# Optimization experiments

Measured on AMD Instinct MI355X. Metric: run time of the kernel, lower is better.

The kernel has to match this reference:

```python
import jax, jax.numpy as jnp
import numpy as np

N, D, M = 100000, 128, 2048


def setup_inputs() -> dict:
    key = jax.random.key(0)
    k1, k2, k3, k4 = jax.random.split(key, 4)
    X = jax.random.normal(k1, (N, D), dtype=jnp.float32)
    Y = jax.random.normal(k2, (N, 1), dtype=jnp.float32)
    centers = jax.random.normal(k3, (M, D), dtype=jnp.float32)
    # alpha is a buffer produced by an inner Falkon solve; use small random values
    alpha = jax.random.normal(k4, (M, 1), dtype=jnp.float32) * 0.01
    sigma = jnp.asarray(1.0, dtype=jnp.float32)     # Gaussian kernel lengthscale (nn.Parameter)
    penalty = jnp.asarray(5.0, dtype=jnp.float32)   # lambda = exp(-penalty)
    return {"X": X, "Y": Y, "centers": centers, "alpha": alpha,
            "sigma": sigma, "penalty": penalty}


def _rbf_mmv(A, B, v, sigma):
    # Gaussian (RBF) kernel mat-vec: exp(-||a-b||^2 / (2 sigma^2)) @ v
    # A:[n,d], B:[m,d], v:[m,1] -> [n,1]
    a2 = jnp.sum(A * A, axis=-1, keepdims=True)          # [n,1]
    b2 = jnp.sum(B * B, axis=-1, keepdims=True).T        # [1,m]
    sq = a2 + b2 - 2.0 * (A @ B.T)                       # [n,m] squared distances
    Kmat = jnp.exp(-sq / (2.0 * sigma * sigma))
    return Kmat @ v


def reference(X, Y, centers, alpha, sigma, penalty):
    # loss = mean((K_NM @ alpha - Y)^2) + exp(-penalty) * alpha^T K_MM alpha
    preds = _rbf_mmv(X, centers, alpha, sigma)                     # [N,1]
    loss = jnp.mean((preds - Y) ** 2)
    pen = jnp.exp(-penalty)
    reg = pen * (alpha.T @ _rbf_mmv(centers, centers, alpha, sigma))  # [1,1]
    total = loss + reg[0, 0]
    return total, preds
```

## Files before the change

### kernel.cpp

```cpp
#include <hip/hip_runtime.h>
#include <stdint.h>

typedef short short8 __attribute__((ext_vector_type(8)));
typedef float f32x4 __attribute__((ext_vector_type(4)));

#define TILE 128

__device__ __forceinline__ unsigned short f32_to_bf16(float f) {
    uint32_t u = __builtin_bit_cast(uint32_t, f);
    u += 0x7FFFu + ((u >> 16) & 1u);
    return (unsigned short)(u >> 16);
}
__device__ __forceinline__ float bf16_to_f32(unsigned short h) {
    return __builtin_bit_cast(float, (uint32_t)h << 16);
}

__global__ void prep_kernel(const float* __restrict__ C,
                            const float* __restrict__ alpha,
                            const float* __restrict__ sigma,
                            unsigned short* __restrict__ Bp,
                            float2* __restrict__ cw)
{
    const int t = threadIdx.x;
    const int g = blockIdx.x;
    const int r = t >> 4;
    const int c16 = t & 15;
    const int R = g * 16 + r;

    const float4* src = (const float4*)(C + (size_t)R * 128 + c16 * 8);
    float4 va = src[0], vb = src[1];
    unsigned short h[8];
    h[0] = f32_to_bf16(va.x); h[1] = f32_to_bf16(va.y);
    h[2] = f32_to_bf16(va.z); h[3] = f32_to_bf16(va.w);
    h[4] = f32_to_bf16(vb.x); h[5] = f32_to_bf16(vb.y);
    h[6] = f32_to_bf16(vb.z); h[7] = f32_to_bf16(vb.w);
    float ss = 0.f;
    #pragma unroll
    for (int k = 0; k < 8; ++k) {
        float f = bf16_to_f32(h[k]);
        ss = fmaf(f, f, ss);
    }
    uint4 pk;
    pk.x = (uint32_t)h[0] | ((uint32_t)h[1] << 16);
    pk.y = (uint32_t)h[2] | ((uint32_t)h[3] << 16);
    pk.z = (uint32_t)h[4] | ((uint32_t)h[5] << 16);
    pk.w = (uint32_t)h[6] | ((uint32_t)h[7] << 16);
    *reinterpret_cast<uint4*>(Bp + (size_t)g * 2048 + c16 * 128 + r * 8) = pk;

    ss += __shfl_xor(ss, 1);
    ss += __shfl_xor(ss, 2);
    ss += __shfl_xor(ss, 4);
    ss += __shfl_xor(ss, 8);
    if (c16 == 0) {
        float sig = sigma[0];
        float q = 0.7213475204444817f / (sig * sig);
        cw[R] = make_float2(ss * q, alpha[R]);
    }
}

__global__ __launch_bounds__(256, 2)
void fused_kernel(const float* __restrict__ X, int N,
                  const float* __restrict__ Yv,
                  const unsigned short* __restrict__ Bp,
                  const float2* __restrict__ cw,
                  const float* __restrict__ alpha,
                  const float* __restrict__ sigma,
                  int nA, int nMt,
                  float* __restrict__ preds_out,
                  float* __restrict__ accLoss,
                  float* __restrict__ accReg)
{
    __shared__ __align__(16) unsigned short ldsA[16384];
    __shared__ float a2p[TILE][2];
    __shared__ float predbuf[TILE][2];

    const int t    = threadIdx.x;
    const int lane = t & 63;
    const int wid  = t >> 6;
    const int wr   = wid >> 1;
    const int wc   = wid & 1;
    const int l15  = lane & 15;
    const int quad = lane >> 4;

    const float sig = sigma[0];
    const float q  = 0.7213475204444817f / (sig * sig);
    const float q2 = 2.0f * q;

    const bool regmode = (int)blockIdx.x >= nA;
    int rowbase;
    float rowterm[4][4];
    const unsigned short* aGlob = nullptr;

    if (!regmode) {
        rowbase = blockIdx.x * TILE;
        const int r_   = t >> 1;
        const int half = t & 1;
        const int grow = rowbase + r_;
        unsigned short* dstbase = ldsA + (r_ >> 4) * 2048 + (r_ & 15) * 8;
        float ss = 0.f;
        if (grow < N) {
            const float4* src = (const float4*)(X + (size_t)grow * 128 + half * 64);
            #pragma unroll
            for (int c = 0; c < 8; ++c) {
                float4 va = src[2 * c], vb = src[2 * c + 1];
                unsigned short h0 = f32_to_bf16(va.x), h1 = f32_to_bf16(va.y);
                unsigned short h2 = f32_to_bf16(va.z), h3 = f32_to_bf16(va.w);
                unsigned short h4 = f32_to_bf16(vb.x), h5 = f32_to_bf16(vb.y);
                unsigned short h6 = f32_to_bf16(vb.z), h7 = f32_to_bf16(vb.w);
                float f0 = bf16_to_f32(h0), f1 = bf16_to_f32(h1);
                float f2 = bf16_to_f32(h2), f3 = bf16_to_f32(h3);
                float f4 = bf16_to_f32(h4), f5 = bf16_to_f32(h5);
                float f6 = bf16_to_f32(h6), f7 = bf16_to_f32(h7);
                ss = fmaf(f0, f0, ss); ss = fmaf(f1, f1, ss);
                ss = fmaf(f2, f2, ss); ss = fmaf(f3, f3, ss);
                ss = fmaf(f4, f4, ss); ss = fmaf(f5, f5, ss);
                ss = fmaf(f6, f6, ss); ss = fmaf(f7, f7, ss);
                uint4 pk;
                pk.x = (uint32_t)h0 | ((uint32_t)h1 << 16);
                pk.y = (uint32_t)h2 | ((uint32_t)h3 << 16);
                pk.z = (uint32_t)h4 | ((uint32_t)h5 << 16);
                pk.w = (uint32_t)h6 | ((uint32_t)h7 << 16);
                *reinterpret_cast<uint4*>(dstbase + (half * 8 + c) * 128) = pk;
            }
        } else {
            uint4 z; z.x = z.y = z.z = z.w = 0u;
            #pragma unroll
            for (int c = 0; c < 8; ++c)
                *reinterpret_cast<uint4*>(dstbase + (half * 8 + c) * 128) = z;
        }
        a2p[r_][half] = ss;
        __syncthreads();
        #pragma unroll
        for (int i = 0; i < 4; ++i)
            #pragma unroll
            for (int r = 0; r < 4; ++r) {
                int rl = wr * 64 + i * 16 + quad * 4 + r;
                rowterm[i][r] = (a2p[rl][0] + a2p[rl][1]) * q;
            }
    } else {
        const int b2 = (int)blockIdx.x - nA;
        rowbase = b2 * TILE;
        aGlob = Bp + (size_t)(b2 * 8 + wr * 4) * 2048 + lane * 8;
        #pragma unroll
        for (int i = 0; i < 4; ++i)
            #pragma unroll
            for (int r = 0; r < 4; ++r)
                rowterm[i][r] = cw[rowbase + wr * 64 + i * 16 + quad * 4 + r].x;
    }

    float srow[4][4] = {};

    for (int mt = 0; mt < nMt; ++mt) {
        const unsigned short* bG = Bp + (size_t)(mt * 8 + wc * 4) * 2048 + lane * 8;
        float2 cj[4];
        #pragma unroll
        for (int j = 0; j < 4; ++j)
            cj[j] = cw[mt * TILE + wc * 64 + j * 16 + l15];

        f32x4 accf[4][4];
        #pragma unroll
        for (int i = 0; i < 4; ++i)
            #pragma unroll
            for (int j = 0; j < 4; ++j)
                accf[i][j] = (f32x4){0.f, 0.f, 0.f, 0.f};

        if (!regmode) {
            const unsigned short* aL = ldsA + (size_t)(wr * 4) * 2048 + lane * 8;
            #pragma unroll
            for (int kk = 0; kk < 4; ++kk) {
                short8 a[4], b[4];
                #pragma unroll
                for (int i = 0; i < 4; ++i)
                    a[i] = *reinterpret_cast<const short8*>(aL + i * 2048 + kk * 512);
                #pragma unroll
                for (int j = 0; j < 4; ++j)
                    b[j] = *reinterpret_cast<const short8*>(bG + j * 2048 + kk * 512);
                #pragma unroll
                for (int i = 0; i < 4; ++i)
                    #pragma unroll
                    for (int j = 0; j < 4; ++j)
                        accf[i][j] = __builtin_amdgcn_mfma_f32_16x16x32_bf16(a[i], b[j], accf[i][j], 0, 0, 0);
            }
        } else {
            #pragma unroll
            for (int kk = 0; kk < 4; ++kk) {
                short8 a[4], b[4];
                #pragma unroll
                for (int i = 0; i < 4; ++i)
                    a[i] = *reinterpret_cast<const short8*>(aGlob + i * 2048 + kk * 512);
                #pragma unroll
                for (int j = 0; j < 4; ++j)
                    b[j] = *reinterpret_cast<const short8*>(bG + j * 2048 + kk * 512);
                #pragma unroll
                for (int i = 0; i < 4; ++i)
                    #pragma unroll
                    for (int j = 0; j < 4; ++j)
                        accf[i][j] = __builtin_amdgcn_mfma_f32_16x16x32_bf16(a[i], b[j], accf[i][j], 0, 0, 0);
            }
        }

        #pragma unroll
        for (int i = 0; i < 4; ++i) {
            #pragma unroll
            for (int r = 0; r < 4; ++r) {
                float nb = rowterm[i][r];
                #pragma unroll
                for (int j = 0; j < 4; ++j) {
                    float u = fmaf(accf[i][j][r], q2, -(nb + cj[j].x));
                    float e = __builtin_amdgcn_exp2f(u);
                    srow[i][r] = fmaf(e, cj[j].y, srow[i][r]);
                }
            }
        }
    }

    #pragma unroll
    for (int i = 0; i < 4; ++i) {
        #pragma unroll
        for (int r = 0; r < 4; ++r) {
            float v = srow[i][r];
            v += __shfl_xor(v, 1);
            v += __shfl_xor(v, 2);
            v += __shfl_xor(v, 4);
            v += __shfl_xor(v, 8);
            if (l15 == 0)
                predbuf[wr * 64 + i * 16 + quad * 4 + r][wc] = v;
        }
    }
    __syncthreads();

    float contrib = 0.f;
    if (t < TILE) {
        int grow = rowbase + t;
        if (!regmode) {
            if (grow < N) {
                float pred = predbuf[t][0] + predbuf[t][1];
                preds_out[grow] = pred;
                float d = pred - Yv[grow];
                contrib = d * d;
            }
        } else {
            float pred = predbuf[t][0] + predbuf[t][1];
            contrib = alpha[grow] * pred;
        }
    }
    contrib += __shfl_xor(contrib, 1);
    contrib += __shfl_xor(contrib, 2);
    contrib += __shfl_xor(contrib, 4);
    contrib += __shfl_xor(contrib, 8);
    contrib += __shfl_xor(contrib, 16);
    contrib += __shfl_xor(contrib, 32);
    if (lane == 0) atomicAdd(regmode ? accReg : accLoss, contrib);
}

__global__ void finalize_kernel(const float* __restrict__ acc,
                                const float* __restrict__ penalty,
                                float* __restrict__ out, float invN)
{
    if (threadIdx.x == 0) {
        out[0] = acc[0] * invN + __expf(-penalty[0]) * acc[1];
    }
}

extern "C" void kernel_launch(void* const* d_in, const int* in_sizes, int n_in,
                              void* d_out, int out_size, void* d_ws, size_t ws_size,
                              hipStream_t stream) {
    const float* X       = (const float*)d_in[0];
    const float* Y       = (const float*)d_in[1];
    const float* centers = (const float*)d_in[2];
    const float* alpha   = (const float*)d_in[3];
    const float* sigma   = (const float*)d_in[4];
    const float* penalty = (const float*)d_in[5];
    float* out = (float*)d_out;

    const int N = in_sizes[1];
    const int M = in_sizes[3];

    unsigned short* Bp = (unsigned short*)d_ws;
    float2* cw = (float2*)((char*)d_ws + (size_t)M * 256);
    float* acc = (float*)((char*)d_ws + (size_t)M * 264);

    hipMemsetAsync(acc, 0, 2 * sizeof(float), stream);

    prep_kernel<<<M / 16, 256, 0, stream>>>(centers, alpha, sigma, Bp, cw);

    const int nA = (N + TILE - 1) / TILE;
    fused_kernel<<<nA + M / TILE, 256, 0, stream>>>(X, N, Y, Bp, cw, alpha, sigma,
                                                    nA, M / TILE, out + 1, acc, acc + 1);

    finalize_kernel<<<1, 64, 0, stream>>>(acc, penalty, out, 1.0f / (float)N);
}
```

Measured before the change: 206.1 us.

## Prefetch B tiles into registers, raise occupancy, fuse memset and finalize into kernels

Loads the next center tile's B fragments into registers during the current tile's compute, a software prefetch meant to hide global load latency. The MFMA loop is reordered per row-block i, so only four accumulators are live at a time, and launch bounds go from 2 to 3 waves. The memset and finalize launches are removed: prep_kernel zeroes the accumulators and the last fused block, found with an atomic counter, writes the final loss. Holding 16 uint4 prefetch registers under a tighter register budget could cause spills.

```diff
diff --git a/kernel.cpp b/kernel.cpp
--- a/kernel.cpp
+++ b/kernel.cpp
@@ -19,13 +19,19 @@
                             const float* __restrict__ alpha,
                             const float* __restrict__ sigma,
                             unsigned short* __restrict__ Bp,
-                            float2* __restrict__ cw)
+                            float2* __restrict__ cw,
+                            float* __restrict__ acc)
 {
     const int t = threadIdx.x;
     const int g = blockIdx.x;
     const int r = t >> 4;
     const int c16 = t & 15;
     const int R = g * 16 + r;
+
+    if (g == 0 && t == 0) {
+        acc[0] = 0.f; acc[1] = 0.f;
+        ((unsigned int*)acc)[2] = 0u;
+    }
 
     const float4* src = (const float4*)(C + (size_t)R * 128 + c16 * 8);
     float4 va = src[0], vb = src[1];
@@ -58,17 +64,18 @@
     }
 }
 
-__global__ __launch_bounds__(256, 2)
+__global__ __launch_bounds__(256, 3)
 void fused_kernel(const float* __restrict__ X, int N,
                   const float* __restrict__ Yv,
                   const unsigned short* __restrict__ Bp,
                   const float2* __restrict__ cw,
                   const float* __restrict__ alpha,
                   const float* __restrict__ sigma,
-                  int nA, int nMt,
+                  const float* __restrict__ penalty,
+                  int nA, int nMt, int nBlk,
                   float* __restrict__ preds_out,
-                  float* __restrict__ accLoss,
-                  float* __restrict__ accReg)
+                  float* __restrict__ out0,
+                  float* __restrict__ acc)
 {
     __shared__ __align__(16) unsigned short ldsA[16384];
     __shared__ float a2p[TILE][2];
@@ -88,8 +95,8 @@
 
     const bool regmode = (int)blockIdx.x >= nA;
     int rowbase;
+    const unsigned short* aGlob = nullptr;
     float rowterm[4][4];
-    const unsigned short* aGlob = nullptr;
 
     if (!regmode) {
         rowbase = blockIdx.x * TILE;
@@ -149,82 +156,78 @@
     }
 
     float srow[4][4] = {};
+    const unsigned short* bbase = Bp + (size_t)(wc * 4) * 2048 + lane * 8;
+    const unsigned short* aLds  = ldsA + (size_t)(wr * 4) * 2048 + lane * 8;
+
+    uint4 braw[16];
+    #pragma unroll
+    for (int kk = 0; kk < 4; ++kk)
+        #pragma unroll
+        for (int j = 0; j < 4; ++j)
+            braw[kk * 4 + j] = *reinterpret_cast<const uint4*>(bbase + (size_t)j * 2048 + kk * 512);
 
     for (int mt = 0; mt < nMt; ++mt) {
-        const unsigned short* bG = Bp + (size_t)(mt * 8 + wc * 4) * 2048 + lane * 8;
         float2 cj[4];
         #pragma unroll
         for (int j = 0; j < 4; ++j)
             cj[j] = cw[mt * TILE + wc * 64 + j * 16 + l15];
 
-        f32x4 accf[4][4];
-        #pragma unroll
-        for (int i = 0; i < 4; ++i)
-            #pragma unroll
-            for (int j = 0; j < 4; ++j)
-                accf[i][j] = (f32x4){0.f, 0.f, 0.f, 0.f};
-
-        if (!regmode) {
-            const unsigned short* aL = ldsA + (size_t)(wr * 4) * 2048 + lane * 8;
-            #pragma unroll
-            for (int kk = 0; kk < 4; ++kk) {
-                short8 a[4], b[4];
-                #pragma unroll
-                for (int i = 0; i < 4; ++i)
-                    a[i] = *reinterpret_cast<const short8*>(aL + i * 2048 + kk * 512);
+        #pragma unroll
+        for (int i = 0; i < 4; ++i) {
+            short8 a[4];
+            if (!regmode) {
+                #pragma unroll
+                for (int kk = 0; kk < 4; ++kk)
+                    a[kk] = *reinterpret_cast<const short8*>(aLds + (size_t)i * 2048 + kk * 512);
+            } else {
+                #pragma unroll
+                for (int kk = 0; kk < 4; ++kk)
+                    a[kk] = *reinterpret_cast<const short8*>(aGlob + (size_t)i * 2048 + kk * 512);
+            }
+            f32x4 acc4[4];
+            #pragma unroll
+            for (int j = 0; j < 4; ++j) acc4[j] = (f32x4){0.f, 0.f, 0.f, 0.f};
+            #pragma unroll
+            for (int kk = 0; kk < 4; ++kk)
                 #pragma unroll
                 for (int j = 0; j < 4; ++j)
-                    b[j] = *reinterpret_cast<const short8*>(bG + j * 2048 + kk * 512);
-                #pragma unroll
-                for (int i = 0; i < 4; ++i)
-                    #pragma unroll
-                    for (int j = 0; j < 4; ++j)
-                        accf[i][j] = __builtin_amdgcn_mfma_f32_16x16x32_bf16(a[i], b[j], accf[i][j], 0, 0, 0);
-            }
-        } else {
-            #pragma unroll
-            for (int kk = 0; kk < 4; ++kk) {
-                short8 a[4], b[4];
-                #pragma unroll
-                for (int i = 0; i < 4; ++i)
-                    a[i] = *reinterpret_cast<const short8*>(aGlob + i * 2048 + kk * 512);
-                #pragma unroll
-                for (int j = 0; j < 4; ++j)
-                    b[j] = *reinterpret_cast<const short8*>(bG + j * 2048 + kk * 512);
-                #pragma unroll
-                for (int i = 0; i < 4; ++i)
-                    #pragma unroll
-                    for (int j = 0; j < 4; ++j)
-                        accf[i][j] = __builtin_amdgcn_mfma_f32_16x16x32_bf16(a[i], b[j], accf[i][j], 0, 0, 0);
-            }
-        }
-
-        #pragma unroll
-        for (int i = 0; i < 4; ++i) {
+                    acc4[j] = __builtin_amdgcn_mfma_f32_16x16x32_bf16(
+                        a[kk], __builtin_bit_cast(short8, braw[kk * 4 + j]), acc4[j], 0, 0, 0);
+
             #pragma unroll
             for (int r = 0; r < 4; ++r) {
                 float nb = rowterm[i][r];
                 #pragma unroll
                 for (int j = 0; j < 4; ++j) {
-                    float u = fmaf(accf[i][j][r], q2, -(nb + cj[j].x));
+                    float u = fmaf(acc4[j][r], q2, -(nb + cj[j].x));
                     float e = __builtin_amdgcn_exp2f(u);
                     srow[i][r] = fmaf(e, cj[j].y, srow[i][r]);
                 }
             }
         }
+
+        if (mt + 1 < nMt) {
+            const unsigned short* bn = bbase + (size_t)(mt + 1) * 8 * 2048;
+            #pragma unroll
+            for (int kk = 0; kk < 4; ++kk)
+                #pragma unroll
+                for (int j = 0; j < 4; ++j)
+                    braw[kk * 4 + j] = *reinterpret_cast<const uint4*>(bn + (size_t)j * 2048 + kk * 512);
+        }
     }
 
     #pragma unroll
     for (int i = 0; i < 4; ++i) {
         #pragma unroll
         for (int r = 0; r < 4; ++r) {
+            int rl = wr * 64 + i * 16 + quad * 4 + r;
             float v = srow[i][r];
             v += __shfl_xor(v, 1);
             v += __shfl_xor(v, 2);
             v += __shfl_xor(v, 4);
             v += __shfl_xor(v, 8);
             if (l15 == 0)
-                predbuf[wr * 64 + i * 16 + quad * 4 + r][wc] = v;
+                predbuf[rl][wc] = v;
         }
     }
     __syncthreads();
@@ -250,15 +253,17 @@
     contrib += __shfl_xor(contrib, 8);
     contrib += __shfl_xor(contrib, 16);
     contrib += __shfl_xor(contrib, 32);
-    if (lane == 0) atomicAdd(regmode ? accReg : accLoss, contrib);
-}
-
-__global__ void finalize_kernel(const float* __restrict__ acc,
-                                const float* __restrict__ penalty,
-                                float* __restrict__ out, float invN)
-{
-    if (threadIdx.x == 0) {
-        out[0] = acc[0] * invN + __expf(-penalty[0]) * acc[1];
+    if (lane == 0) atomicAdd(regmode ? (acc + 1) : (acc + 0), contrib);
+
+    __syncthreads();
+    if (t == 0) {
+        __threadfence();
+        unsigned int old = atomicAdd((unsigned int*)(acc + 2), 1u);
+        if (old == (unsigned int)(nBlk - 1)) {
+            float lv = atomicAdd(acc + 0, 0.0f);
+            float rv = atomicAdd(acc + 1, 0.0f);
+            out0[0] = lv / (float)N + __expf(-penalty[0]) * rv;
+        }
     }
 }
 
@@ -280,13 +285,11 @@
     float2* cw = (float2*)((char*)d_ws + (size_t)M * 256);
     float* acc = (float*)((char*)d_ws + (size_t)M * 264);
 
-    hipMemsetAsync(acc, 0, 2 * sizeof(float), stream);
-
-    prep_kernel<<<M / 16, 256, 0, stream>>>(centers, alpha, sigma, Bp, cw);
-
-    const int nA = (N + TILE - 1) / TILE;
-    fused_kernel<<<nA + M / TILE, 256, 0, stream>>>(X, N, Y, Bp, cw, alpha, sigma,
-                                                    nA, M / TILE, out + 1, acc, acc + 1);
-
-    finalize_kernel<<<1, 64, 0, stream>>>(acc, penalty, out, 1.0f / (float)N);
-}
+    prep_kernel<<<M / 16, 256, 0, stream>>>(centers, alpha, sigma, Bp, cw, acc);
+
+    const int nA  = (N + TILE - 1) / TILE;
+    const int nMt = M / TILE;
+    const int nBlk = nA + nMt;
+    fused_kernel<<<nBlk, 256, 0, stream>>>(X, N, Y, Bp, cw, alpha, sigma, penalty,
+                                           nA, nMt, nBlk, out + 1, out, acc);
+}
```

After: 304.4 us. 47.7% more time.
